# Kernel optimization log

Hardware: AMD Instinct MI355X
Metric: run time of the kernel (lower is better)

## Reference

```python
import jax, jax.numpy as jnp
import numpy as np
import math

B, S, D, H = 2, 2048, 2048, 16
HD = D // H  # 128
EPS = 1e-5


def setup_inputs() -> dict:
    key = jax.random.key(0)
    ks = jax.random.split(key, 8)
    s = 0.02
    return {
        "x": jax.random.normal(ks[0], (B, S, D), jnp.float32),
        "ln1_s": jnp.ones((D,), jnp.float32),
        "ln1_b": jnp.zeros((D,), jnp.float32),
        "Wq": jax.random.normal(ks[1], (D, D), jnp.float32) * s,
        "Wk": jax.random.normal(ks[2], (D, D), jnp.float32) * s,
        "Wv": jax.random.normal(ks[3], (D, D), jnp.float32) * s,
        "Wo": jax.random.normal(ks[4], (D, D), jnp.float32) * s,
        "bo": jnp.zeros((D,), jnp.float32),
        "ln2_s": jnp.ones((D,), jnp.float32),
        "ln2_b": jnp.zeros((D,), jnp.float32),
        "W1": jax.random.normal(ks[5], (D, 4 * D), jnp.float32) * s,
        "b1": jnp.zeros((4 * D,), jnp.float32),
        "W2": jax.random.normal(ks[6], (4 * D, D), jnp.float32) * s,
        "b2": jnp.zeros((D,), jnp.float32),
    }


def _layernorm(x, scale, shift):
    mean = jnp.mean(x, axis=-1, keepdims=True)
    var = jnp.var(x, axis=-1, keepdims=True)  # unbiased=False
    return scale * (x - mean) * jax.lax.rsqrt(var + EPS) + shift


def _gelu_tanh(x):
    c = math.sqrt(2.0 / math.pi)
    return 0.5 * x * (1.0 + jnp.tanh(c * (x + 0.044715 * x * x * x)))


def reference(x, ln1_s, ln1_b, Wq, Wk, Wv, Wo, bo, ln2_s, ln2_b, W1, b1, W2, b2):
    b, n, d = x.shape
    # --- pre-norm MHA ---
    xn = _layernorm(x, ln1_s, ln1_b)
    q = (xn @ Wq).reshape(b, n, H, HD)
    k = (xn @ Wk).reshape(b, n, H, HD)
    v = (xn @ Wv).reshape(b, n, H, HD)
    scores = jnp.einsum("bqhd,bkhd->bhqk", q, k) / math.sqrt(HD)
    causal = jnp.tril(jnp.ones((n, n), bool))  # True = keep
    scores = jnp.where(causal, scores, -jnp.inf)
    attn = jax.nn.softmax(scores, axis=-1)
    ctx = jnp.einsum("bhqk,bkhd->bqhd", attn, v).reshape(b, n, d)
    attn_out = ctx @ Wo + bo
    x = x + attn_out
    # --- pre-norm FFN ---
    xn2 = _layernorm(x, ln2_s, ln2_b)
    h = _gelu_tanh(xn2 @ W1 + b1)
    ff_out = h @ W2 + b2
    return x + ff_out
```

## Files before the change

### kernel.cpp

```cpp
#include <hip/hip_runtime.h>

typedef unsigned short u16;
typedef __attribute__((ext_vector_type(8))) short short8;
typedef __attribute__((ext_vector_type(8))) __bf16 bf16x8;
typedef __attribute__((ext_vector_type(4))) float f32x4;

#define DEV __device__ __forceinline__

DEV float bf2f(u16 u) {
    union { unsigned v; float f; } x; x.v = ((unsigned)u) << 16; return x.f;
}
DEV u16 f2bf(float f) {
    union { float f; unsigned v; } x; x.f = f;
    unsigned r = x.v + 0x7fff + ((x.v >> 16) & 1);
    return (u16)(r >> 16);
}

DEV f32x4 mfma16(short8 a, short8 b, f32x4 c) {
    return __builtin_amdgcn_mfma_f32_16x16x32_bf16(
        __builtin_bit_cast(bf16x8, a), __builtin_bit_cast(bf16x8, b), c, 0, 0, 0);
}

typedef const __attribute__((address_space(1))) void* gas_ptr;
typedef __attribute__((address_space(3))) void* las_ptr;

__global__ __launch_bounds__(256) void transpose_kernel(
    const float* __restrict__ in, u16* __restrict__ out, int R, int C)
{
    __shared__ u16 t[64][65];
    int tid = threadIdx.x;
    int bc = blockIdx.x * 64, br = blockIdx.y * 64;
    int r = tid >> 2, cs = (tid & 3) * 16;
    const float* ip = in + (size_t)(br + r) * C + bc + cs;
    f32x4 v0 = *(const f32x4*)ip, v1 = *(const f32x4*)(ip + 4),
          v2 = *(const f32x4*)(ip + 8), v3 = *(const f32x4*)(ip + 12);
#pragma unroll
    for (int j = 0; j < 4; j++) {
        t[r][cs + j]      = f2bf(v0[j]);
        t[r][cs + 4 + j]  = f2bf(v1[j]);
        t[r][cs + 8 + j]  = f2bf(v2[j]);
        t[r][cs + 12 + j] = f2bf(v3[j]);
    }
    __syncthreads();
    int n = tid >> 2, ks = (tid & 3) * 16;
    short8 o0, o1;
#pragma unroll
    for (int j = 0; j < 8; j++) { o0[j] = (short)t[ks + j][n]; o1[j] = (short)t[ks + 8 + j][n]; }
    u16* op = out + (size_t)(bc + n) * R + br + ks;
    *(short8*)op = o0;
    *(short8*)(op + 8) = o1;
}

template<int INBF>
__global__ __launch_bounds__(256) void ln_kernel(
    const void* __restrict__ xp, const float* __restrict__ sc, const float* __restrict__ sh,
    u16* __restrict__ out)
{
    int row = blockIdx.x, tid = threadIdx.x;
    float f[8], sum = 0.f, ss = 0.f;
    if (INBF) {
        short8 v = *(const short8*)((const u16*)xp + (size_t)row * 2048 + tid * 8);
#pragma unroll
        for (int j = 0; j < 8; j++) f[j] = bf2f((u16)v[j]);
    } else {
        const f32x4* xr = (const f32x4*)((const float*)xp + (size_t)row * 2048 + tid * 8);
        f32x4 a = xr[0], b = xr[1];
#pragma unroll
        for (int j = 0; j < 4; j++) { f[j] = a[j]; f[4 + j] = b[j]; }
    }
#pragma unroll
    for (int j = 0; j < 8; j++) { sum += f[j]; ss += f[j] * f[j]; }
#pragma unroll
    for (int m = 1; m < 64; m <<= 1) { sum += __shfl_xor(sum, m, 64); ss += __shfl_xor(ss, m, 64); }
    __shared__ float red[8];
    int w = tid >> 6, l = tid & 63;
    if (l == 0) { red[w] = sum; red[4 + w] = ss; }
    __syncthreads();
    sum = red[0] + red[1] + red[2] + red[3];
    ss  = red[4] + red[5] + red[6] + red[7];
    float mean = sum * (1.f / 2048.f);
    float var  = ss * (1.f / 2048.f) - mean * mean;
    float rstd = rsqrtf(var + 1e-5f);
    const f32x4* sp = (const f32x4*)(sc + tid * 8);
    const f32x4* bp = (const f32x4*)(sh + tid * 8);
    f32x4 s0 = sp[0], s1 = sp[1], b0 = bp[0], b1 = bp[1];
    short8 o;
#pragma unroll
    for (int j = 0; j < 4; j++) {
        o[j]     = (short)f2bf((f[j] - mean) * rstd * s0[j] + b0[j]);
        o[4 + j] = (short)f2bf((f[4 + j] - mean) * rstd * s1[j] + b1[j]);
    }
    *(short8*)(out + (size_t)row * 2048 + tid * 8) = o;
}

template<int EPI, int OUTF, int RESBF, int SPLITM>
__global__ __launch_bounds__(256, 2) void gemm_bt(
    const u16* __restrict__ A, const u16* __restrict__ BT, void* __restrict__ Cp,
    const float* __restrict__ bias, const void* __restrict__ res, int M, int N, int K)
{
    __shared__ u16 As[2][128 * 32];
    __shared__ u16 Bs[2][128 * 32];
    int tid = threadIdx.x, l = tid & 63, w = tid >> 6;
    int mbase = blockIdx.y * 128, nbase = blockIdx.x * 128;
    int NK = K >> 5;
    const u16* Ag = A + (size_t)mbase * K;
    const u16* Bg = BT + (size_t)nbase * K;

    auto stage = [&](const u16* G, u16* Ld, int kt) {
#pragma unroll
        for (int c = 0; c < 2; c++) {
            int slot = c * 256 + w * 64 + l;
            const u16* g = G + (size_t)(slot >> 2) * K + kt * 32 + (slot & 3) * 8;
            __builtin_amdgcn_global_load_lds((gas_ptr)g, (las_ptr)(Ld + (c * 256 + w * 64) * 8), 16, 0, 0);
        }
    };

    f32x4 acc[4][4];
#pragma unroll
    for (int i = 0; i < 4; i++)
#pragma unroll
        for (int j = 0; j < 4; j++) acc[i][j] = (f32x4){0.f, 0.f, 0.f, 0.f};
    int wr = (w >> 1) * 64, wc = (w & 1) * 64;

    stage(Ag, As[0], 0);
    stage(Bg, Bs[0], 0);
    __syncthreads();
    int buf = 0;
    for (int kt = 0; kt < NK; ++kt) {
        if (kt + 1 < NK) { stage(Ag, As[buf ^ 1], kt + 1); stage(Bg, Bs[buf ^ 1], kt + 1); }
        short8 af[4], bfr[4];
#pragma unroll
        for (int i = 0; i < 4; i++) {
            af[i]  = *(const short8*)&As[buf][(wr + i * 16 + (l & 15)) * 32 + (l >> 4) * 8];
            bfr[i] = *(const short8*)&Bs[buf][(wc + i * 16 + (l & 15)) * 32 + (l >> 4) * 8];
        }
#pragma unroll
        for (int mi = 0; mi < 4; mi++)
#pragma unroll
            for (int ni = 0; ni < 4; ni++)
                acc[mi][ni] = mfma16(af[mi], bfr[ni], acc[mi][ni]);
        __syncthreads();
        buf ^= 1;
    }

#pragma unroll
    for (int mi = 0; mi < 4; mi++) {
#pragma unroll
        for (int ni = 0; ni < 4; ni++) {
            int col = nbase + wc + ni * 16 + (l & 15);
            float bval = (EPI != 0) ? bias[col] : 0.f;
#pragma unroll
            for (int r = 0; r < 4; r++) {
                int row = mbase + wr + mi * 16 + (l >> 4) * 4 + r;
                float v = acc[mi][ni][r];
                if (EPI == 1) {
                    size_t ridx = (size_t)row * N + col;
                    float rv = RESBF ? bf2f(((const u16*)res)[ridx]) : ((const float*)res)[ridx];
                    v += bval + rv;
                }
                if (EPI == 2) {
                    v += bval;
                    float t = tanhf(0.7978845608028654f * (v + 0.044715f * v * v * v));
                    v = 0.5f * v * (1.f + t);
                }
                if (SPLITM == 1) {
                    ((u16*)Cp)[(size_t)(col >> 11) * 8388608ULL + (size_t)row * 2048 + (col & 2047)] = f2bf(v);
                } else if (SPLITM == 2) {
                    ((u16*)Cp)[(size_t)(col >> 11) * 4194304ULL + (size_t)row * 2048 + (col & 2047)] = f2bf(v);
                } else if (OUTF) {
                    ((float*)Cp)[(size_t)row * N + col] = v;
                } else {
                    ((u16*)Cp)[(size_t)row * N + col] = f2bf(v);
                }
            }
        }
    }
}

__global__ __launch_bounds__(256, 2) void attn_kernel(
    const u16* __restrict__ Q, const u16* __restrict__ Kp, const u16* __restrict__ VTg,
    u16* __restrict__ O)
{
    __shared__ u16 Ks[64 * 128];
    __shared__ u16 VT[128 * 64];
    __shared__ u16 Ps[4 * 2048];
    int tid = threadIdx.x, l = tid & 63, w = tid >> 6;
    int qtl = (int)gridDim.x - 1 - (int)blockIdx.x;
    int bh = blockIdx.y, b = bh >> 4, h = bh & 15;
    const float SCALE = 0.08838834764831845f;
    int qbase = qtl * 128;
    size_t bS = (size_t)b * 2048;
    const u16* vrow = VTg + (size_t)bh * 128 * 2048;

    short8 qf[2][4];
#pragma unroll
    for (int mg = 0; mg < 2; mg++) {
        int qrow = qbase + w * 32 + mg * 16 + (l & 15);
        const u16* qp = Q + (bS + qrow) * 2048 + h * 128 + (l >> 4) * 8;
#pragma unroll
        for (int ds = 0; ds < 4; ds++) qf[mg][ds] = *(const short8*)(qp + ds * 32);
    }
    float m_[2][4], l_[2][4];
    f32x4 o_[2][8];
#pragma unroll
    for (int mg = 0; mg < 2; mg++)
#pragma unroll
        for (int r = 0; r < 4; r++) { m_[mg][r] = -1e30f; l_[mg][r] = 0.f; }
#pragma unroll
    for (int mg = 0; mg < 2; mg++)
#pragma unroll
        for (int d = 0; d < 8; d++) o_[mg][d] = (f32x4){0.f, 0.f, 0.f, 0.f};

    int ktmax = 2 * qtl + 1;
    for (int kt = 0; kt <= ktmax; ++kt) {
        int kbase = kt * 64;
#pragma unroll
        for (int it = 0; it < 4; ++it) {
            int slot = it * 256 + tid;
            int key = slot >> 4, dseg = slot & 15;
            short8 kv = *(const short8*)(Kp + (bS + kbase + key) * 2048 + h * 128 + dseg * 8);
            int kidx = ((key * 256 + dseg * 16) ^ ((key & 7) << 4)) >> 1;
            *(short8*)&Ks[kidx] = kv;
            int d = slot >> 3, k8 = slot & 7;
            short8 vv = *(const short8*)(vrow + (size_t)d * 2048 + kbase + k8 * 8);
            int vidx = ((d * 128 + k8 * 16) ^ ((d & 7) << 4)) >> 1;
            *(short8*)&VT[vidx] = vv;
        }
        __syncthreads();

        f32x4 s[2][4];
#pragma unroll
        for (int mg = 0; mg < 2; mg++)
#pragma unroll
            for (int kg = 0; kg < 4; kg++) s[mg][kg] = (f32x4){0.f, 0.f, 0.f, 0.f};
        __builtin_amdgcn_s_setprio(1);
#pragma unroll
        for (int kg = 0; kg < 4; kg++) {
            int key0 = kg * 16 + (l & 15);
#pragma unroll
            for (int ds = 0; ds < 4; ds++) {
                int i0 = ((key0 * 256 + ds * 64 + (l >> 4) * 16) ^ ((key0 & 7) << 4)) >> 1;
                short8 kb = *(const short8*)&Ks[i0];
                s[0][kg] = mfma16(qf[0][ds], kb, s[0][kg]);
                s[1][kg] = mfma16(qf[1][ds], kb, s[1][kg]);
            }
        }
        __builtin_amdgcn_s_setprio(0);

        bool domask = (kbase + 63) > qbase;
        float alpha[2][4];
        u16* Pw = &Ps[w * 2048];
#pragma unroll
        for (int mg = 0; mg < 2; mg++) {
#pragma unroll
            for (int r = 0; r < 4; r++) {
                int qrow = qbase + w * 32 + mg * 16 + (l >> 4) * 4 + r;
                float aa[4];
#pragma unroll
                for (int kg = 0; kg < 4; kg++) {
                    float a = s[mg][kg][r] * SCALE;
                    if (domask && (kbase + kg * 16 + (l & 15)) > qrow) a = -1e30f;
                    aa[kg] = a;
                }
                float mx = fmaxf(fmaxf(aa[0], aa[1]), fmaxf(aa[2], aa[3]));
                mx = fmaxf(mx, __shfl_xor(mx, 1, 64));
                mx = fmaxf(mx, __shfl_xor(mx, 2, 64));
                mx = fmaxf(mx, __shfl_xor(mx, 4, 64));
                mx = fmaxf(mx, __shfl_xor(mx, 8, 64));
                float mn = fmaxf(m_[mg][r], mx);
                float al = __expf(m_[mg][r] - mn);
                m_[mg][r] = mn;
                float p[4], rs = 0.f;
#pragma unroll
                for (int kg = 0; kg < 4; kg++) { p[kg] = __expf(aa[kg] - mn); rs += p[kg]; }
                rs += __shfl_xor(rs, 1, 64);
                rs += __shfl_xor(rs, 2, 64);
                rs += __shfl_xor(rs, 4, 64);
                rs += __shfl_xor(rs, 8, 64);
                l_[mg][r] = l_[mg][r] * al + rs;
                alpha[mg][r] = al;
#pragma unroll
                for (int kg = 0; kg < 4; kg++) {
                    int col = kg * 16 + (l & 15);
                    int lp = ((l >> 4) * 4 + r) | (((col >> 3) & 3) << 4);
                    Pw[(mg * 2 + (col >> 5)) * 512 + lp * 8 + (col & 7)] = f2bf(p[kg]);
                }
            }
        }
#pragma unroll
        for (int mg = 0; mg < 2; mg++)
#pragma unroll
            for (int dblk = 0; dblk < 8; dblk++)
#pragma unroll
                for (int r = 0; r < 4; r++) o_[mg][dblk][r] *= alpha[mg][r];

        __builtin_amdgcn_s_setprio(1);
#pragma unroll
        for (int kk = 0; kk < 2; kk++) {
            short8 pa0 = *(const short8*)&Pw[(0 * 2 + kk) * 512 + l * 8];
            short8 pa1 = *(const short8*)&Pw[(1 * 2 + kk) * 512 + l * 8];
#pragma unroll
            for (int dblk = 0; dblk < 8; dblk++) {
                int d = dblk * 16 + (l & 15);
                int iv = ((d * 128 + kk * 64 + (l >> 4) * 16) ^ ((d & 7) << 4)) >> 1;
                short8 vb = *(const short8*)&VT[iv];
                o_[0][dblk] = mfma16(pa0, vb, o_[0][dblk]);
                o_[1][dblk] = mfma16(pa1, vb, o_[1][dblk]);
            }
        }
        __builtin_amdgcn_s_setprio(0);
        __syncthreads();
    }

#pragma unroll
    for (int mg = 0; mg < 2; mg++) {
#pragma unroll
        for (int dblk = 0; dblk < 8; dblk++) {
#pragma unroll
            for (int r = 0; r < 4; r++) {
                int qrow = qbase + w * 32 + mg * 16 + (l >> 4) * 4 + r;
                float v = o_[mg][dblk][r] / l_[mg][r];
                O[(bS + qrow) * 2048 + h * 128 + dblk * 16 + (l & 15)] = f2bf(v);
            }
        }
    }
}

extern "C" void kernel_launch(void* const* d_in, const int* in_sizes, int n_in,
                              void* d_out, int out_size, void* d_ws, size_t ws_size,
                              hipStream_t stream)
{
    const float* x    = (const float*)d_in[0];
    const float* ln1s = (const float*)d_in[1];
    const float* ln1b = (const float*)d_in[2];
    const float* Wq   = (const float*)d_in[3];
    const float* Wk   = (const float*)d_in[4];
    const float* Wv   = (const float*)d_in[5];
    const float* Wo   = (const float*)d_in[6];
    const float* bo   = (const float*)d_in[7];
    const float* ln2s = (const float*)d_in[8];
    const float* ln2b = (const float*)d_in[9];
    const float* W1   = (const float*)d_in[10];
    const float* b1   = (const float*)d_in[11];
    const float* W2   = (const float*)d_in[12];
    const float* b2   = (const float*)d_in[13];
    float* out = (float*)d_out;
    const size_t ACT = 8388608ULL;

    u16* ws16 = (u16*)d_ws;
    u16* xn   = ws16;
    u16* q    = ws16 + ACT;
    u16* k    = ws16 + 2 * ACT;
    u16* vT   = ws16 + 3 * ACT;
    u16* hbuf = ws16 + 2 * ACT;
    u16* wt   = ws16 + 6 * ACT;
    u16* x2   = q;

    dim3 blk(256);
    transpose_kernel<<<dim3(32, 32), blk, 0, stream>>>(Wq, wt,                  2048, 2048);
    transpose_kernel<<<dim3(32, 32), blk, 0, stream>>>(Wk, wt + (ACT >> 1),     2048, 2048);
    transpose_kernel<<<dim3(32, 32), blk, 0, stream>>>(Wv, wt + ACT,            2048, 2048);
    transpose_kernel<<<dim3(32, 32), blk, 0, stream>>>(Wo, wt + 3 * (ACT >> 1), 2048, 2048);
    ln_kernel<0><<<4096, blk, 0, stream>>>(x, ln1s, ln1b, xn);
    gemm_bt<0, 0, 0, 1><<<dim3(32, 32), blk, 0, stream>>>(xn, wt, q, nullptr, nullptr, 4096, 4096, 2048);
    gemm_bt<0, 0, 0, 2><<<dim3(32, 16), blk, 0, stream>>>(wt + ACT, xn, vT, nullptr, nullptr, 2048, 4096, 2048);
    attn_kernel<<<dim3(16, 32), blk, 0, stream>>>(q, k, vT, xn);
    gemm_bt<1, 0, 0, 0><<<dim3(16, 32), blk, 0, stream>>>(xn, wt + 3 * (ACT >> 1), x2, bo, x, 4096, 2048, 2048);
    transpose_kernel<<<dim3(128, 32), blk, 0, stream>>>(W1, wt, 2048, 8192);
    ln_kernel<1><<<4096, blk, 0, stream>>>(x2, ln2s, ln2b, xn);
    gemm_bt<2, 0, 0, 0><<<dim3(64, 32), blk, 0, stream>>>(xn, wt, hbuf, b1, nullptr, 4096, 8192, 2048);
    transpose_kernel<<<dim3(32, 128), blk, 0, stream>>>(W2, wt, 8192, 2048);
    gemm_bt<1, 1, 1, 0><<<dim3(16, 32), blk, 0, stream>>>(hbuf, wt, out, b2, x2, 4096, 2048, 8192);
}
```

Baseline: 739.1 us.

## Replace 128x128 GEMM with 8-wave 256-wide tiles, 4-stage pipeline, swizzled LDS

Replaces the 4-wave 128x128 double-buffered GEMM with a 512-thread kernel using 256xBM tiles, a 4-slot LDS ring with 3 tiles in flight, explicit vmcnt waits and raw barriers. LDS layout is XOR-swizzled to avoid bank conflicts, workgroups are remapped for L2 locality, and MFMA issue runs at raised priority. The aim is more data reuse per tile and better latency hiding in every GEMM. In exchange it uses much more LDS per block and relies on hand-counted vmcnt values, which may cut occupancy or break if the load counts change.

```diff
diff --git a/kernel.cpp b/kernel.cpp
--- a/kernel.cpp
+++ b/kernel.cpp
@@ -93,65 +93,113 @@
     *(short8*)(out + (size_t)row * 2048 + tid * 8) = o;
 }
 
-template<int EPI, int OUTF, int RESBF, int SPLITM>
-__global__ __launch_bounds__(256, 2) void gemm_bt(
+template<int ROWS>
+DEV void stage_op(const u16* __restrict__ G, int ldK, int t, u16* lds_op, int tid)
+{
+#pragma unroll
+    for (int c2 = 0; c2 < ROWS / 128; c2++) {
+        int ci = c2 * 512 + tid;
+        int r = ci >> 2, chp = ci & 3;
+        int ch = chp ^ ((r >> 1) & 3);
+        const u16* g = G + (size_t)r * ldK + t * 32 + ch * 8;
+        u16* d = lds_op + (c2 * 512 + (tid >> 6) * 64) * 8;
+        __builtin_amdgcn_global_load_lds((gas_ptr)g, (las_ptr)d, 16, 0, 0);
+    }
+}
+
+DEV short8 read_frag(const u16* lds_op, int r, int ch)
+{
+    int off = r * 32 + ((ch ^ ((r >> 1) & 3)) << 3);
+    return *(const short8*)(lds_op + off);
+}
+
+template<int BM, int EPI, int OUTF, int RESBF, int SPLITM>
+__global__ __launch_bounds__(512, 2) void gemm8(
     const u16* __restrict__ A, const u16* __restrict__ BT, void* __restrict__ Cp,
     const float* __restrict__ bias, const void* __restrict__ res, int M, int N, int K)
 {
-    __shared__ u16 As[2][128 * 32];
-    __shared__ u16 Bs[2][128 * 32];
+    constexpr int MI = BM / 32;
+    constexpr int LPG = (BM == 256) ? 4 : 3;
+    __shared__ u16 As[4][BM * 32];
+    __shared__ u16 Bs[4][256 * 32];
+
     int tid = threadIdx.x, l = tid & 63, w = tid >> 6;
-    int mbase = blockIdx.y * 128, nbase = blockIdx.x * 128;
-    int NK = K >> 5;
+    int wm = w >> 2, wn = w & 3;
+
+    int nbx = gridDim.x, nby = gridDim.y;
+    int nwg = nbx * nby;
+    int orig = blockIdx.y * nbx + blockIdx.x;
+    int wg = (orig & 7) * (nwg >> 3) + (orig >> 3);
+    int bx = wg / nby, by = wg % nby;
+
+    int mbase = by * BM, nbase = bx * 256;
     const u16* Ag = A + (size_t)mbase * K;
     const u16* Bg = BT + (size_t)nbase * K;
-
-    auto stage = [&](const u16* G, u16* Ld, int kt) {
-#pragma unroll
-        for (int c = 0; c < 2; c++) {
-            int slot = c * 256 + w * 64 + l;
-            const u16* g = G + (size_t)(slot >> 2) * K + kt * 32 + (slot & 3) * 8;
-            __builtin_amdgcn_global_load_lds((gas_ptr)g, (las_ptr)(Ld + (c * 256 + w * 64) * 8), 16, 0, 0);
-        }
-    };
-
-    f32x4 acc[4][4];
-#pragma unroll
-    for (int i = 0; i < 4; i++)
+    int NT = K >> 5;
+
+#pragma unroll
+    for (int t0 = 0; t0 < 3; t0++) {
+        stage_op<BM>(Ag, K, t0, As[t0], tid);
+        stage_op<256>(Bg, K, t0, Bs[t0], tid);
+    }
+    if constexpr (LPG == 4) asm volatile("s_waitcnt vmcnt(8)" ::: "memory");
+    else                    asm volatile("s_waitcnt vmcnt(6)" ::: "memory");
+    __builtin_amdgcn_sched_barrier(0);
+    __builtin_amdgcn_s_barrier();
+    __builtin_amdgcn_sched_barrier(0);
+
+    f32x4 acc[MI][4];
+#pragma unroll
+    for (int i = 0; i < MI; i++)
 #pragma unroll
         for (int j = 0; j < 4; j++) acc[i][j] = (f32x4){0.f, 0.f, 0.f, 0.f};
-    int wr = (w >> 1) * 64, wc = (w & 1) * 64;
-
-    stage(Ag, As[0], 0);
-    stage(Bg, Bs[0], 0);
-    __syncthreads();
-    int buf = 0;
-    for (int kt = 0; kt < NK; ++kt) {
-        if (kt + 1 < NK) { stage(Ag, As[buf ^ 1], kt + 1); stage(Bg, Bs[buf ^ 1], kt + 1); }
-        short8 af[4], bfr[4];
-#pragma unroll
-        for (int i = 0; i < 4; i++) {
-            af[i]  = *(const short8*)&As[buf][(wr + i * 16 + (l & 15)) * 32 + (l >> 4) * 8];
-            bfr[i] = *(const short8*)&Bs[buf][(wc + i * 16 + (l & 15)) * 32 + (l >> 4) * 8];
-        }
-#pragma unroll
-        for (int mi = 0; mi < 4; mi++)
-#pragma unroll
-            for (int ni = 0; ni < 4; ni++)
-                acc[mi][ni] = mfma16(af[mi], bfr[ni], acc[mi][ni]);
-        __syncthreads();
-        buf ^= 1;
-    }
-
-#pragma unroll
-    for (int mi = 0; mi < 4; mi++) {
+
+    for (int t = 0; t < NT; ++t) {
+        int slot = t & 3;
+        if (t + 3 < NT) {
+            int ps = (t + 3) & 3;
+            stage_op<BM>(Ag, K, t + 3, As[ps], tid);
+            stage_op<256>(Bg, K, t + 3, Bs[ps], tid);
+        }
+        short8 af[MI], bf[4];
+#pragma unroll
+        for (int i = 0; i < MI; i++)
+            af[i] = read_frag(As[slot], wm * (BM / 2) + i * 16 + (l & 15), l >> 4);
+#pragma unroll
+        for (int j = 0; j < 4; j++)
+            bf[j] = read_frag(Bs[slot], wn * 64 + j * 16 + (l & 15), l >> 4);
+        __builtin_amdgcn_s_setprio(1);
+#pragma unroll
+        for (int i = 0; i < MI; i++)
+#pragma unroll
+            for (int j = 0; j < 4; j++)
+                acc[i][j] = mfma16(af[i], bf[j], acc[i][j]);
+        __builtin_amdgcn_s_setprio(0);
+        if (t < NT - 1) {
+            if (t + 3 < NT) {
+                if constexpr (LPG == 4) asm volatile("s_waitcnt vmcnt(8)" ::: "memory");
+                else                    asm volatile("s_waitcnt vmcnt(6)" ::: "memory");
+            } else if (t + 2 < NT) {
+                if constexpr (LPG == 4) asm volatile("s_waitcnt vmcnt(4)" ::: "memory");
+                else                    asm volatile("s_waitcnt vmcnt(3)" ::: "memory");
+            } else {
+                asm volatile("s_waitcnt vmcnt(0)" ::: "memory");
+            }
+            __builtin_amdgcn_sched_barrier(0);
+            __builtin_amdgcn_s_barrier();
+            __builtin_amdgcn_sched_barrier(0);
+        }
+    }
+
+#pragma unroll
+    for (int mi = 0; mi < MI; mi++) {
 #pragma unroll
         for (int ni = 0; ni < 4; ni++) {
-            int col = nbase + wc + ni * 16 + (l & 15);
+            int col = nbase + wn * 64 + ni * 16 + (l & 15);
             float bval = (EPI != 0) ? bias[col] : 0.f;
 #pragma unroll
             for (int r = 0; r < 4; r++) {
-                int row = mbase + wr + mi * 16 + (l >> 4) * 4 + r;
+                int row = mbase + wm * (BM / 2) + mi * 16 + (l >> 4) * 4 + r;
                 float v = acc[mi][ni][r];
                 if (EPI == 1) {
                     size_t ridx = (size_t)row * N + col;
@@ -160,8 +208,8 @@
                 }
                 if (EPI == 2) {
                     v += bval;
-                    float t = tanhf(0.7978845608028654f * (v + 0.044715f * v * v * v));
-                    v = 0.5f * v * (1.f + t);
+                    float tt = tanhf(0.7978845608028654f * (v + 0.044715f * v * v * v));
+                    v = 0.5f * v * (1.f + tt);
                 }
                 if (SPLITM == 1) {
                     ((u16*)Cp)[(size_t)(col >> 11) * 8388608ULL + (size_t)row * 2048 + (col & 2047)] = f2bf(v);
@@ -355,20 +403,21 @@
     u16* hbuf = ws16 + 2 * ACT;
     u16* wt   = ws16 + 6 * ACT;
     u16* x2   = q;
-
-    dim3 blk(256);
+    (void)k;
+
+    dim3 blk(256), blk8(512);
     transpose_kernel<<<dim3(32, 32), blk, 0, stream>>>(Wq, wt,                  2048, 2048);
     transpose_kernel<<<dim3(32, 32), blk, 0, stream>>>(Wk, wt + (ACT >> 1),     2048, 2048);
     transpose_kernel<<<dim3(32, 32), blk, 0, stream>>>(Wv, wt + ACT,            2048, 2048);
     transpose_kernel<<<dim3(32, 32), blk, 0, stream>>>(Wo, wt + 3 * (ACT >> 1), 2048, 2048);
     ln_kernel<0><<<4096, blk, 0, stream>>>(x, ln1s, ln1b, xn);
-    gemm_bt<0, 0, 0, 1><<<dim3(32, 32), blk, 0, stream>>>(xn, wt, q, nullptr, nullptr, 4096, 4096, 2048);
-    gemm_bt<0, 0, 0, 2><<<dim3(32, 16), blk, 0, stream>>>(wt + ACT, xn, vT, nullptr, nullptr, 2048, 4096, 2048);
+    gemm8<256, 0, 0, 0, 1><<<dim3(16, 16), blk8, 0, stream>>>(xn, wt, q, nullptr, nullptr, 4096, 4096, 2048);
+    gemm8<128, 0, 0, 0, 2><<<dim3(16, 16), blk8, 0, stream>>>(wt + ACT, xn, vT, nullptr, nullptr, 2048, 4096, 2048);
     attn_kernel<<<dim3(16, 32), blk, 0, stream>>>(q, k, vT, xn);
-    gemm_bt<1, 0, 0, 0><<<dim3(16, 32), blk, 0, stream>>>(xn, wt + 3 * (ACT >> 1), x2, bo, x, 4096, 2048, 2048);
+    gemm8<128, 1, 0, 0, 0><<<dim3(8, 32), blk8, 0, stream>>>(xn, wt + 3 * (ACT >> 1), x2, bo, x, 4096, 2048, 2048);
     transpose_kernel<<<dim3(128, 32), blk, 0, stream>>>(W1, wt, 2048, 8192);
     ln_kernel<1><<<4096, blk, 0, stream>>>(x2, ln2s, ln2b, xn);
-    gemm_bt<2, 0, 0, 0><<<dim3(64, 32), blk, 0, stream>>>(xn, wt, hbuf, b1, nullptr, 4096, 8192, 2048);
+    gemm8<256, 2, 0, 0, 0><<<dim3(32, 16), blk8, 0, stream>>>(xn, wt, hbuf, b1, nullptr, 4096, 8192, 2048);
     transpose_kernel<<<dim3(32, 128), blk, 0, stream>>>(W2, wt, 8192, 2048);
-    gemm_bt<1, 1, 1, 0><<<dim3(16, 32), blk, 0, stream>>>(hbuf, wt, out, b2, x2, 4096, 2048, 8192);
-}
+    gemm8<128, 1, 1, 1, 0><<<dim3(8, 32), blk8, 0, stream>>>(hbuf, wt, out, b2, x2, 4096, 2048, 8192);
+}
```

Result: slower. 832.3 us (+12.6%).

## Rewrite GEMM with 256x128 tiles, triple-buffered swizzled LDS, and XCD-aware block remap

Applied to the files above, without the earlier changes.

Replaces the 128x128, BK=32 double-buffered GEMM with a 512-thread kernel computing 256x128 tiles at BK=64 using a three-stage LDS ring, so loads run two k-steps ahead. LDS chunks are XOR-swizzled to avoid bank conflicts, fragment reads are split in two halves with MFMA priority raised via setprio, and waits use explicit vmcnt counts. Block indices are remapped so consecutive tiles land on the same XCD for better L2 reuse. It uses 144KB of LDS per block, which limits occupancy, and the hand-tuned waitcnt logic is fragile.

```diff
diff --git a/kernel.cpp b/kernel.cpp
--- a/kernel.cpp
+++ b/kernel.cpp
@@ -94,24 +94,40 @@
 }
 
 template<int EPI, int OUTF, int RESBF, int SPLITM>
-__global__ __launch_bounds__(256, 2) void gemm_bt(
+__global__ __launch_bounds__(512, 2) void gemm3r(
     const u16* __restrict__ A, const u16* __restrict__ BT, void* __restrict__ Cp,
     const float* __restrict__ bias, const void* __restrict__ res, int M, int N, int K)
 {
-    __shared__ u16 As[2][128 * 32];
-    __shared__ u16 Bs[2][128 * 32];
+    __shared__ u16 As[3][256 * 64];
+    __shared__ u16 Bs[3][128 * 64];
     int tid = threadIdx.x, l = tid & 63, w = tid >> 6;
-    int mbase = blockIdx.y * 128, nbase = blockIdx.x * 128;
-    int NK = K >> 5;
+    int wm = w >> 1, wn = w & 1;
+
+    int nbx = gridDim.x, nby = gridDim.y;
+    int nwg = nbx * nby;
+    int orig = blockIdx.y * nbx + blockIdx.x;
+    int wg = (orig & 7) * (nwg >> 3) + (orig >> 3);
+    int bx = wg / nby, by = wg % nby;
+
+    int mbase = by * 256, nbase = bx * 128;
     const u16* Ag = A + (size_t)mbase * K;
     const u16* Bg = BT + (size_t)nbase * K;
-
-    auto stage = [&](const u16* G, u16* Ld, int kt) {
-#pragma unroll
-        for (int c = 0; c < 2; c++) {
-            int slot = c * 256 + w * 64 + l;
-            const u16* g = G + (size_t)(slot >> 2) * K + kt * 32 + (slot & 3) * 8;
-            __builtin_amdgcn_global_load_lds((gas_ptr)g, (las_ptr)(Ld + (c * 256 + w * 64) * 8), 16, 0, 0);
+    int NT = K >> 6;
+
+    auto stage = [&](int s, int u) {
+#pragma unroll
+        for (int g = 0; g < 4; g++) {
+            int ci = g * 512 + tid;
+            int r = ci >> 3, ch = (ci & 7) ^ (r & 7);
+            const u16* gp = Ag + (size_t)r * K + u * 64 + ch * 8;
+            __builtin_amdgcn_global_load_lds((gas_ptr)gp, (las_ptr)&As[s][(g * 512 + w * 64) * 8], 16, 0, 0);
+        }
+#pragma unroll
+        for (int g = 0; g < 2; g++) {
+            int ci = g * 512 + tid;
+            int r = ci >> 3, ch = (ci & 7) ^ (r & 7);
+            const u16* gp = Bg + (size_t)r * K + u * 64 + ch * 8;
+            __builtin_amdgcn_global_load_lds((gas_ptr)gp, (las_ptr)&Bs[s][(g * 512 + w * 64) * 8], 16, 0, 0);
         }
     };
 
@@ -120,38 +136,80 @@
     for (int i = 0; i < 4; i++)
 #pragma unroll
         for (int j = 0; j < 4; j++) acc[i][j] = (f32x4){0.f, 0.f, 0.f, 0.f};
-    int wr = (w >> 1) * 64, wc = (w & 1) * 64;
-
-    stage(Ag, As[0], 0);
-    stage(Bg, Bs[0], 0);
-    __syncthreads();
-    int buf = 0;
-    for (int kt = 0; kt < NK; ++kt) {
-        if (kt + 1 < NK) { stage(Ag, As[buf ^ 1], kt + 1); stage(Bg, Bs[buf ^ 1], kt + 1); }
-        short8 af[4], bfr[4];
+
+    stage(0, 0);
+    stage(1, 1);
+    asm volatile("s_waitcnt vmcnt(6)" ::: "memory");
+    __builtin_amdgcn_sched_barrier(0);
+    __builtin_amdgcn_s_barrier();
+    __builtin_amdgcn_sched_barrier(0);
+
+    int s0 = 0, s1 = 1, s2 = 2;
+    for (int u = 0; u < NT; ++u) {
+        if (u + 2 < NT) stage(s2, u + 2);
+        const u16* Abase = &As[s0][0];
+        const u16* Bbase = &Bs[s0][0];
+        short8 a0[4], b0[4], a1[4], b1[4];
+        int ra = wm * 64 + (l & 15);
+        int rb = wn * 64 + (l & 15);
+        int c0 = (l >> 4), c1 = 4 + (l >> 4);
 #pragma unroll
         for (int i = 0; i < 4; i++) {
-            af[i]  = *(const short8*)&As[buf][(wr + i * 16 + (l & 15)) * 32 + (l >> 4) * 8];
-            bfr[i] = *(const short8*)&Bs[buf][(wc + i * 16 + (l & 15)) * 32 + (l >> 4) * 8];
-        }
-#pragma unroll
-        for (int mi = 0; mi < 4; mi++)
-#pragma unroll
-            for (int ni = 0; ni < 4; ni++)
-                acc[mi][ni] = mfma16(af[mi], bfr[ni], acc[mi][ni]);
-        __syncthreads();
-        buf ^= 1;
+            int r = ra + i * 16;
+            a0[i] = *(const short8*)&Abase[r * 64 + ((c0 ^ (r & 7)) << 3)];
+        }
+#pragma unroll
+        for (int j = 0; j < 4; j++) {
+            int r = rb + j * 16;
+            b0[j] = *(const short8*)&Bbase[r * 64 + ((c0 ^ (r & 7)) << 3)];
+        }
+        asm volatile("s_waitcnt lgkmcnt(0)" ::: "memory");
+#pragma unroll
+        for (int i = 0; i < 4; i++) {
+            int r = ra + i * 16;
+            a1[i] = *(const short8*)&Abase[r * 64 + ((c1 ^ (r & 7)) << 3)];
+        }
+#pragma unroll
+        for (int j = 0; j < 4; j++) {
+            int r = rb + j * 16;
+            b1[j] = *(const short8*)&Bbase[r * 64 + ((c1 ^ (r & 7)) << 3)];
+        }
+        __builtin_amdgcn_sched_barrier(0);
+        __builtin_amdgcn_s_setprio(1);
+#pragma unroll
+        for (int i = 0; i < 4; i++)
+#pragma unroll
+            for (int j = 0; j < 4; j++)
+                acc[i][j] = mfma16(a0[i], b0[j], acc[i][j]);
+        __builtin_amdgcn_s_setprio(0);
+        asm volatile("s_waitcnt lgkmcnt(0)" ::: "memory");
+        __builtin_amdgcn_sched_barrier(0);
+        __builtin_amdgcn_s_setprio(1);
+#pragma unroll
+        for (int i = 0; i < 4; i++)
+#pragma unroll
+            for (int j = 0; j < 4; j++)
+                acc[i][j] = mfma16(a1[i], b1[j], acc[i][j]);
+        __builtin_amdgcn_s_setprio(0);
+        if (u < NT - 1) {
+            if (u + 2 < NT) asm volatile("s_waitcnt vmcnt(6)" ::: "memory");
+            else            asm volatile("s_waitcnt vmcnt(0)" ::: "memory");
+            __builtin_amdgcn_sched_barrier(0);
+            __builtin_amdgcn_s_barrier();
+            __builtin_amdgcn_sched_barrier(0);
+        }
+        int t = s0; s0 = s1; s1 = s2; s2 = t;
     }
 
 #pragma unroll
     for (int mi = 0; mi < 4; mi++) {
 #pragma unroll
         for (int ni = 0; ni < 4; ni++) {
-            int col = nbase + wc + ni * 16 + (l & 15);
+            int col = nbase + wn * 64 + ni * 16 + (l & 15);
             float bval = (EPI != 0) ? bias[col] : 0.f;
 #pragma unroll
             for (int r = 0; r < 4; r++) {
-                int row = mbase + wr + mi * 16 + (l >> 4) * 4 + r;
+                int row = mbase + wm * 64 + mi * 16 + (l >> 4) * 4 + r;
                 float v = acc[mi][ni][r];
                 if (EPI == 1) {
                     size_t ridx = (size_t)row * N + col;
@@ -160,8 +218,8 @@
                 }
                 if (EPI == 2) {
                     v += bval;
-                    float t = tanhf(0.7978845608028654f * (v + 0.044715f * v * v * v));
-                    v = 0.5f * v * (1.f + t);
+                    float tt = tanhf(0.7978845608028654f * (v + 0.044715f * v * v * v));
+                    v = 0.5f * v * (1.f + tt);
                 }
                 if (SPLITM == 1) {
                     ((u16*)Cp)[(size_t)(col >> 11) * 8388608ULL + (size_t)row * 2048 + (col & 2047)] = f2bf(v);
@@ -355,20 +413,21 @@
     u16* hbuf = ws16 + 2 * ACT;
     u16* wt   = ws16 + 6 * ACT;
     u16* x2   = q;
-
-    dim3 blk(256);
+    (void)k;
+
+    dim3 blk(256), blk8(512);
     transpose_kernel<<<dim3(32, 32), blk, 0, stream>>>(Wq, wt,                  2048, 2048);
     transpose_kernel<<<dim3(32, 32), blk, 0, stream>>>(Wk, wt + (ACT >> 1),     2048, 2048);
     transpose_kernel<<<dim3(32, 32), blk, 0, stream>>>(Wv, wt + ACT,            2048, 2048);
     transpose_kernel<<<dim3(32, 32), blk, 0, stream>>>(Wo, wt + 3 * (ACT >> 1), 2048, 2048);
     ln_kernel<0><<<4096, blk, 0, stream>>>(x, ln1s, ln1b, xn);
-    gemm_bt<0, 0, 0, 1><<<dim3(32, 32), blk, 0, stream>>>(xn, wt, q, nullptr, nullptr, 4096, 4096, 2048);
-    gemm_bt<0, 0, 0, 2><<<dim3(32, 16), blk, 0, stream>>>(wt + ACT, xn, vT, nullptr, nullptr, 2048, 4096, 2048);
+    gemm3r<0, 0, 0, 1><<<dim3(32, 16), blk8, 0, stream>>>(xn, wt, q, nullptr, nullptr, 4096, 4096, 2048);
+    gemm3r<0, 0, 0, 2><<<dim3(32, 8), blk8, 0, stream>>>(wt + ACT, xn, vT, nullptr, nullptr, 2048, 4096, 2048);
     attn_kernel<<<dim3(16, 32), blk, 0, stream>>>(q, k, vT, xn);
-    gemm_bt<1, 0, 0, 0><<<dim3(16, 32), blk, 0, stream>>>(xn, wt + 3 * (ACT >> 1), x2, bo, x, 4096, 2048, 2048);
+    gemm3r<1, 0, 0, 0><<<dim3(16, 16), blk8, 0, stream>>>(xn, wt + 3 * (ACT >> 1), x2, bo, x, 4096, 2048, 2048);
     transpose_kernel<<<dim3(128, 32), blk, 0, stream>>>(W1, wt, 2048, 8192);
     ln_kernel<1><<<4096, blk, 0, stream>>>(x2, ln2s, ln2b, xn);
-    gemm_bt<2, 0, 0, 0><<<dim3(64, 32), blk, 0, stream>>>(xn, wt, hbuf, b1, nullptr, 4096, 8192, 2048);
+    gemm3r<2, 0, 0, 0><<<dim3(64, 16), blk8, 0, stream>>>(xn, wt, hbuf, b1, nullptr, 4096, 8192, 2048);
     transpose_kernel<<<dim3(32, 128), blk, 0, stream>>>(W2, wt, 8192, 2048);
-    gemm_bt<1, 1, 1, 0><<<dim3(16, 32), blk, 0, stream>>>(hbuf, wt, out, b2, x2, 4096, 2048, 8192);
-}
+    gemm3r<1, 1, 1, 0><<<dim3(16, 16), blk8, 0, stream>>>(hbuf, wt, out, b2, x2, 4096, 2048, 8192);
+}
```

New measurement: 783.3 us. 1.06x slower.

## Deepen GEMM K-tile to 64 with XOR-swizzled LDS, XCD-aware block remap, setprio

Applied to the files above, without the earlier changes.

Replaces the GEMM kernel with a version that stages 64-wide K tiles instead of 32, halving the number of barriers and loop iterations per K. The LDS layout is XOR-swizzled by row so fragment reads avoid bank conflicts. Workgroup IDs are remapped so consecutive tiles land on the same XCD (chunks of grid/8), grouping blocks that share B or A panels for L2 reuse. MFMA bursts are wrapped in s_setprio. LDS use doubles to 64KB per block, which may limit occupancy to two blocks per CU.

```diff
diff --git a/kernel.cpp b/kernel.cpp
--- a/kernel.cpp
+++ b/kernel.cpp
@@ -93,25 +93,37 @@
     *(short8*)(out + (size_t)row * 2048 + tid * 8) = o;
 }
 
-template<int EPI, int OUTF, int RESBF, int SPLITM>
-__global__ __launch_bounds__(256, 2) void gemm_bt(
+template<int EPI, int OUTF, int RESBF, int SPLITM, int SHAREB>
+__global__ __launch_bounds__(256, 2) void gemm_bt2(
     const u16* __restrict__ A, const u16* __restrict__ BT, void* __restrict__ Cp,
     const float* __restrict__ bias, const void* __restrict__ res, int M, int N, int K)
 {
-    __shared__ u16 As[2][128 * 32];
-    __shared__ u16 Bs[2][128 * 32];
+    __shared__ u16 As[2][128 * 64];
+    __shared__ u16 Bs[2][128 * 64];
     int tid = threadIdx.x, l = tid & 63, w = tid >> 6;
-    int mbase = blockIdx.y * 128, nbase = blockIdx.x * 128;
-    int NK = K >> 5;
+
+    int nbx = gridDim.x, nby = gridDim.y;
+    int nwg = nbx * nby;
+    int orig = blockIdx.y * nbx + blockIdx.x;
+    int nch = nwg >> 3;
+    int wg = (orig & 7) * nch + (orig >> 3);
+    int bx, by;
+    if (SHAREB) { bx = wg / nby; by = wg % nby; }
+    else        { by = wg / nbx; bx = wg % nbx; }
+
+    int mbase = by * 128, nbase = bx * 128;
     const u16* Ag = A + (size_t)mbase * K;
     const u16* Bg = BT + (size_t)nbase * K;
-
-    auto stage = [&](const u16* G, u16* Ld, int kt) {
-#pragma unroll
-        for (int c = 0; c < 2; c++) {
-            int slot = c * 256 + w * 64 + l;
-            const u16* g = G + (size_t)(slot >> 2) * K + kt * 32 + (slot & 3) * 8;
-            __builtin_amdgcn_global_load_lds((gas_ptr)g, (las_ptr)(Ld + (c * 256 + w * 64) * 8), 16, 0, 0);
+    int NT = K >> 6;
+
+    auto stage = [&](const u16* G, u16* Ld, int t) {
+#pragma unroll
+        for (int g = 0; g < 4; g++) {
+            int ci = g * 256 + tid;
+            int r = ci >> 3, chp = ci & 7;
+            int ch = chp ^ (r & 7);
+            const u16* gp = G + (size_t)r * K + t * 64 + ch * 8;
+            __builtin_amdgcn_global_load_lds((gas_ptr)gp, (las_ptr)(Ld + (g * 256 + w * 64) * 8), 16, 0, 0);
         }
     };
 
@@ -122,23 +134,32 @@
         for (int j = 0; j < 4; j++) acc[i][j] = (f32x4){0.f, 0.f, 0.f, 0.f};
     int wr = (w >> 1) * 64, wc = (w & 1) * 64;
 
-    stage(Ag, As[0], 0);
-    stage(Bg, Bs[0], 0);
+    stage(Ag, As[0], 0); stage(Bg, Bs[0], 0);
     __syncthreads();
     int buf = 0;
-    for (int kt = 0; kt < NK; ++kt) {
-        if (kt + 1 < NK) { stage(Ag, As[buf ^ 1], kt + 1); stage(Bg, Bs[buf ^ 1], kt + 1); }
-        short8 af[4], bfr[4];
-#pragma unroll
-        for (int i = 0; i < 4; i++) {
-            af[i]  = *(const short8*)&As[buf][(wr + i * 16 + (l & 15)) * 32 + (l >> 4) * 8];
-            bfr[i] = *(const short8*)&Bs[buf][(wc + i * 16 + (l & 15)) * 32 + (l >> 4) * 8];
-        }
-#pragma unroll
-        for (int mi = 0; mi < 4; mi++)
-#pragma unroll
-            for (int ni = 0; ni < 4; ni++)
-                acc[mi][ni] = mfma16(af[mi], bfr[ni], acc[mi][ni]);
+    for (int t = 0; t < NT; ++t) {
+        if (t + 1 < NT) { stage(Ag, As[buf ^ 1], t + 1); stage(Bg, Bs[buf ^ 1], t + 1); }
+        short8 af[2][4], bfr[2][4];
+#pragma unroll
+        for (int ks = 0; ks < 2; ks++) {
+            int c = ks * 4 + (l >> 4);
+#pragma unroll
+            for (int i = 0; i < 4; i++) {
+                int ra = wr + i * 16 + (l & 15);
+                af[ks][i] = *(const short8*)&As[buf][ra * 64 + ((c ^ (ra & 7)) << 3)];
+                int rb = wc + i * 16 + (l & 15);
+                bfr[ks][i] = *(const short8*)&Bs[buf][rb * 64 + ((c ^ (rb & 7)) << 3)];
+            }
+        }
+        __builtin_amdgcn_s_setprio(1);
+#pragma unroll
+        for (int ks = 0; ks < 2; ks++)
+#pragma unroll
+            for (int mi = 0; mi < 4; mi++)
+#pragma unroll
+                for (int ni = 0; ni < 4; ni++)
+                    acc[mi][ni] = mfma16(af[ks][mi], bfr[ks][ni], acc[mi][ni]);
+        __builtin_amdgcn_s_setprio(0);
         __syncthreads();
         buf ^= 1;
     }
@@ -160,8 +181,8 @@
                 }
                 if (EPI == 2) {
                     v += bval;
-                    float t = tanhf(0.7978845608028654f * (v + 0.044715f * v * v * v));
-                    v = 0.5f * v * (1.f + t);
+                    float tt = tanhf(0.7978845608028654f * (v + 0.044715f * v * v * v));
+                    v = 0.5f * v * (1.f + tt);
                 }
                 if (SPLITM == 1) {
                     ((u16*)Cp)[(size_t)(col >> 11) * 8388608ULL + (size_t)row * 2048 + (col & 2047)] = f2bf(v);
@@ -355,6 +376,7 @@
     u16* hbuf = ws16 + 2 * ACT;
     u16* wt   = ws16 + 6 * ACT;
     u16* x2   = q;
+    (void)k;
 
     dim3 blk(256);
     transpose_kernel<<<dim3(32, 32), blk, 0, stream>>>(Wq, wt,                  2048, 2048);
@@ -362,13 +384,13 @@
     transpose_kernel<<<dim3(32, 32), blk, 0, stream>>>(Wv, wt + ACT,            2048, 2048);
     transpose_kernel<<<dim3(32, 32), blk, 0, stream>>>(Wo, wt + 3 * (ACT >> 1), 2048, 2048);
     ln_kernel<0><<<4096, blk, 0, stream>>>(x, ln1s, ln1b, xn);
-    gemm_bt<0, 0, 0, 1><<<dim3(32, 32), blk, 0, stream>>>(xn, wt, q, nullptr, nullptr, 4096, 4096, 2048);
-    gemm_bt<0, 0, 0, 2><<<dim3(32, 16), blk, 0, stream>>>(wt + ACT, xn, vT, nullptr, nullptr, 2048, 4096, 2048);
+    gemm_bt2<0, 0, 0, 1, 1><<<dim3(32, 32), blk, 0, stream>>>(xn, wt, q, nullptr, nullptr, 4096, 4096, 2048);
+    gemm_bt2<0, 0, 0, 2, 1><<<dim3(32, 16), blk, 0, stream>>>(wt + ACT, xn, vT, nullptr, nullptr, 2048, 4096, 2048);
     attn_kernel<<<dim3(16, 32), blk, 0, stream>>>(q, k, vT, xn);
-    gemm_bt<1, 0, 0, 0><<<dim3(16, 32), blk, 0, stream>>>(xn, wt + 3 * (ACT >> 1), x2, bo, x, 4096, 2048, 2048);
+    gemm_bt2<1, 0, 0, 0, 0><<<dim3(16, 32), blk, 0, stream>>>(xn, wt + 3 * (ACT >> 1), x2, bo, x, 4096, 2048, 2048);
     transpose_kernel<<<dim3(128, 32), blk, 0, stream>>>(W1, wt, 2048, 8192);
     ln_kernel<1><<<4096, blk, 0, stream>>>(x2, ln2s, ln2b, xn);
-    gemm_bt<2, 0, 0, 0><<<dim3(64, 32), blk, 0, stream>>>(xn, wt, hbuf, b1, nullptr, 4096, 8192, 2048);
+    gemm_bt2<2, 0, 0, 0, 1><<<dim3(64, 32), blk, 0, stream>>>(xn, wt, hbuf, b1, nullptr, 4096, 8192, 2048);
     transpose_kernel<<<dim3(32, 128), blk, 0, stream>>>(W2, wt, 8192, 2048);
-    gemm_bt<1, 1, 1, 0><<<dim3(16, 32), blk, 0, stream>>>(hbuf, wt, out, b2, x2, 4096, 2048, 8192);
-}
+    gemm_bt2<1, 1, 1, 0, 0><<<dim3(16, 32), blk, 0, stream>>>(hbuf, wt, out, b2, x2, 4096, 2048, 8192);
+}
```

Measured after the change: 669.9 us. -9.4%, faster.
